# Kernel tuning notes

Measured on AMD Instinct MI355X. Metric: run time of the kernel, lower is better.

## Reference

```python
import jax, jax.numpy as jnp
import numpy as np

C, H, W = 1024, 128, 128

def setup_inputs() -> dict:
    key = jax.random.key(0)
    k1, k2 = jax.random.split(key)
    x = jax.random.normal(k1, (C, H, W), dtype=jnp.float32)
    gamma = jax.random.normal(k2, (1,), dtype=jnp.float32)
    return {"x": x, "gamma": gamma}

def reference(x, gamma):
    c, h, w = x.shape
    q = x.reshape(c, h * w)                      # (C, HW)
    energy = jnp.matmul(q, q.T)                  # (C, C)
    # negated-energy softmax: softmax(max(energy) - energy) along last dim
    energy_new = jnp.max(energy, axis=-1, keepdims=True) - energy
    attention = jax.nn.softmax(energy_new, axis=-1)
    out = jnp.matmul(attention, q).reshape(c, h, w)
    return gamma * out + x
```

## Files before the change

kernel.cpp:

```cpp
#include <hip/hip_runtime.h>
#include <hip/hip_bf16.h>

typedef unsigned short u16;
typedef float  f32x16 __attribute__((ext_vector_type(16)));
typedef short  bf16x8 __attribute__((ext_vector_type(8)));
typedef u16    u16x8  __attribute__((ext_vector_type(8)));

#define CDIM 1024
#define HW   16384

typedef const void __attribute__((address_space(1))) gvoid;
typedef void __attribute__((address_space(3))) svoid;

__device__ __forceinline__ u16 f2bf(float f) {
    unsigned u = __float_as_uint(f);
    u += 0x7fffu + ((u >> 16) & 1u);
    return (u16)(u >> 16);
}
__device__ __forceinline__ float bf2f(u16 h) { return __uint_as_float(((unsigned)h) << 16); }

__device__ __forceinline__ f32x16 mfma32(bf16x8 a, bf16x8 b, f32x16 c) {
    return __builtin_amdgcn_mfma_f32_32x32x16_bf16(a, b, c, 0, 0, 0);
}

__global__ __launch_bounds__(256) void k_convert(const float* __restrict__ x,
                                                 u16* __restrict__ hi, u16* __restrict__ lo,
                                                 u16* __restrict__ hiT)
{
    __shared__ u16 tile[64][72];
    const int pb = blockIdx.x;
    const int cb = blockIdx.y;
    const int tid = threadIdx.x;
#pragma unroll
    for (int pass = 0; pass < 4; ++pass) {
        const int i  = (tid >> 4) + (pass << 4);
        const int j4 = (tid & 15) << 2;
        const long gidx = (long)(cb * 64 + i) * HW + pb * 64 + j4;
        const float4 v = *(const float4*)(x + gidx);
        ushort4 h, l;
        h.x = f2bf(v.x); l.x = f2bf(v.x - bf2f(h.x));
        h.y = f2bf(v.y); l.y = f2bf(v.y - bf2f(h.y));
        h.z = f2bf(v.z); l.z = f2bf(v.z - bf2f(h.z));
        h.w = f2bf(v.w); l.w = f2bf(v.w - bf2f(h.w));
        *(ushort4*)(hi + gidx) = h;
        *(ushort4*)(lo + gidx) = l;
        tile[i][j4 + 0] = h.x; tile[i][j4 + 1] = h.y;
        tile[i][j4 + 2] = h.z; tile[i][j4 + 3] = h.w;
    }
    __syncthreads();
#pragma unroll
    for (int pass = 0; pass < 2; ++pass) {
        const int j  = (tid >> 3) + (pass << 5);
        const int c8 = (tid & 7) << 3;
        u16x8 v;
#pragma unroll
        for (int q = 0; q < 8; ++q) v[q] = tile[c8 + q][j];
        *(u16x8*)(hiT + (long)(pb * 64 + j) * CDIM + cb * 64 + c8) = v;
    }
}

__device__ __forceinline__ void stage_half(const u16* __restrict__ gbase, long ldg,
                                           int rowhalf, int ktile, u16* seg, int tid)
{
    const int lane = tid & 63;
    const int wv   = tid >> 6;
    const int s    = lane >> 3;
    const int r7   = (lane & 7) ^ s;
    const int col  = s << 3;
#pragma unroll
    for (int q = 0; q < 2; ++q) {
        const int j = wv + (q << 3);
        const u16* src = gbase + (long)((rowhalf << 7) + (j << 3) + r7) * ldg
                               + (ktile << 6) + col;
        __builtin_amdgcn_global_load_lds((gvoid*)src, (svoid*)(seg + (j << 9)), 16, 0, 0);
    }
}

__device__ __forceinline__ bf16x8 rd_frag(const u16* seg, int row, int kk, int lane)
{
    const int s = (kk << 1) + (lane >> 5);
    const int off = ((row >> 3) << 9) + (s << 6) + (((row & 7) ^ s) << 3);
    return *(const bf16x8*)(seg + off);
}

#define SBAR()  do { __builtin_amdgcn_sched_barrier(0); \
                     __builtin_amdgcn_s_barrier();      \
                     __builtin_amdgcn_sched_barrier(0); } while (0)

template<int EPI>
__global__ __launch_bounds__(512, 2) void k_gemm8(
    const u16* __restrict__ Amat, const u16* __restrict__ Bhi, const u16* __restrict__ Blo,
    long lda, long ldb, int kchunk, int nbn,
    float* __restrict__ C, long ldc, long csplit,
    const float* __restrict__ X, const float* __restrict__ gamma)
{
    __shared__ u16 sA[2][2][8192];
    __shared__ u16 sB[2][2][8192];

    const int tid  = threadIdx.x;
    const int lane = tid & 63;
    const int w    = tid >> 6;
    const int wm   = w >> 2;
    const int wn   = w & 3;
    const int l31  = lane & 31;

    const int ks   = blockIdx.y;
    const int nblk = gridDim.x;
    const int lin  = blockIdx.x;
    const int ti   = (lin & 7) * (nblk >> 3) + (lin >> 3);
    const int bi   = ti / nbn, bn = ti % nbn;

    const u16* Ab = Amat + (long)bi * 256 * lda + (long)ks * kchunk;
    const u16* Bb;
    if (EPI == 0) {
        const int half = nbn >> 1;
        Bb = (bn < half) ? (Bhi + (long)bn * 256 * ldb)
                         : (Blo + (long)(bn - half) * 256 * ldb);
    } else {
        Bb = Bhi + (long)bn * 256 * ldb;
    }
    Bb += (long)ks * kchunk;

    const int nkt = kchunk >> 6;

    f32x16 acc[4][2];
    {
        f32x16 z;
#pragma unroll
        for (int r = 0; r < 16; ++r) z[r] = 0.f;
#pragma unroll
        for (int f = 0; f < 4; ++f)
#pragma unroll
            for (int g = 0; g < 2; ++g) acc[f][g] = z;
    }

    stage_half(Ab, lda, 0, 0, sA[0][0], tid);
    stage_half(Ab, lda, 1, 0, sA[0][1], tid);
    stage_half(Bb, ldb, 0, 0, sB[0][0], tid);
    stage_half(Bb, ldb, 1, 0, sB[0][1], tid);

    for (int u = 0; u < nkt; ++u) {
        const int db = u & 1;

        SBAR();

        if (u + 1 < nkt) {
            stage_half(Ab, lda, 0, u + 1, sA[db ^ 1][0], tid);
            stage_half(Ab, lda, 1, u + 1, sA[db ^ 1][1], tid);
            stage_half(Bb, ldb, 0, u + 1, sB[db ^ 1][0], tid);
            stage_half(Bb, ldb, 1, u + 1, sB[db ^ 1][1], tid);
            asm volatile("s_waitcnt vmcnt(8)" ::: "memory");
        } else {
            asm volatile("s_waitcnt vmcnt(0)" ::: "memory");
        }

        bf16x8 A0f[2][4], B0f[4], B1f[4];
#pragma unroll
        for (int f = 0; f < 2; ++f)
#pragma unroll
            for (int kk = 0; kk < 4; ++kk)
                A0f[f][kk] = rd_frag(sA[db][0], wm * 64 + f * 32 + l31, kk, lane);
#pragma unroll
        for (int kk = 0; kk < 4; ++kk) B0f[kk] = rd_frag(sB[db][0], wn * 32 + l31, kk, lane);
#pragma unroll
        for (int kk = 0; kk < 4; ++kk) B1f[kk] = rd_frag(sB[db][1], wn * 32 + l31, kk, lane);

        __builtin_amdgcn_s_setprio(1);
#pragma unroll
        for (int kk = 0; kk < 4; ++kk) {
            acc[0][0] = mfma32(A0f[0][kk], B0f[kk], acc[0][0]);
            acc[1][0] = mfma32(A0f[1][kk], B0f[kk], acc[1][0]);
        }
#pragma unroll
        for (int kk = 0; kk < 4; ++kk) {
            acc[0][1] = mfma32(A0f[0][kk], B1f[kk], acc[0][1]);
            acc[1][1] = mfma32(A0f[1][kk], B1f[kk], acc[1][1]);
        }
        __builtin_amdgcn_s_setprio(0);

        bf16x8 A1f[2][4];
#pragma unroll
        for (int f = 0; f < 2; ++f)
#pragma unroll
            for (int kk = 0; kk < 4; ++kk)
                A1f[f][kk] = rd_frag(sA[db][1], wm * 64 + f * 32 + l31, kk, lane);

        __builtin_amdgcn_s_setprio(1);
#pragma unroll
        for (int kk = 0; kk < 4; ++kk) {
            acc[2][1] = mfma32(A1f[0][kk], B1f[kk], acc[2][1]);
            acc[3][1] = mfma32(A1f[1][kk], B1f[kk], acc[3][1]);
        }
#pragma unroll
        for (int kk = 0; kk < 4; ++kk) {
            acc[2][0] = mfma32(A1f[0][kk], B0f[kk], acc[2][0]);
            acc[3][0] = mfma32(A1f[1][kk], B0f[kk], acc[3][0]);
        }
        __builtin_amdgcn_s_setprio(0);
    }

    if (EPI == 0) {
        float* Cb = C + (long)ks * csplit;
#pragma unroll
        for (int f = 0; f < 4; ++f)
#pragma unroll
            for (int g = 0; g < 2; ++g)
#pragma unroll
                for (int r = 0; r < 16; ++r) {
                    const int row = bi * 256 + (f >> 1) * 128 + wm * 64 + (f & 1) * 32
                                    + (r & 3) + ((r >> 2) << 3) + ((lane >> 5) << 2);
                    const int col = bn * 256 + g * 128 + wn * 32 + l31;
                    Cb[(long)row * ldc + col] = acc[f][g][r];
                }
    } else {
        const float gm = gamma[0];
#pragma unroll
        for (int f = 0; f < 4; ++f)
#pragma unroll
            for (int g = 0; g < 2; ++g)
#pragma unroll
                for (int r = 0; r < 16; ++r) {
                    const int row = bi * 256 + (f >> 1) * 128 + wm * 64 + (f & 1) * 32
                                    + (r & 3) + ((r >> 2) << 3) + ((lane >> 5) << 2);
                    const int col = bn * 256 + g * 128 + wn * 32 + l31;
                    const long idx = (long)row * ldc + col;
                    C[idx] = gm * acc[f][g][r] + X[idx];
                }
    }
}

__global__ __launch_bounds__(256) void k_symmetrize(const float* __restrict__ E12,
                                                    float* __restrict__ Esym)
{
    __shared__ float tr[64][65];
    const int jb = blockIdx.x, ib = blockIdx.y, tid = threadIdx.x;
    float4 accv[4];
#pragma unroll
    for (int e4 = 0; e4 < 4; ++e4) {
        const int e = tid + (e4 << 8);
        const int i = e >> 4, j4 = (e & 15) << 2;
        float ax = 0, ay = 0, az = 0, aw = 0, bx = 0, by = 0, bz = 0, bw = 0;
#pragma unroll
        for (int ks = 0; ks < 8; ++ks) {
            const float* base = E12 + (long)ks * (1024 * 2048);
            float4 p1 = *(const float4*)(base + (long)(ib * 64 + i) * 2048 + jb * 64 + j4);
            float4 p2 = *(const float4*)(base + (long)(ib * 64 + i) * 2048 + 1024 + jb * 64 + j4);
            float4 p3 = *(const float4*)(base + (long)(jb * 64 + i) * 2048 + 1024 + ib * 64 + j4);
            ax += p1.x + p2.x; ay += p1.y + p2.y; az += p1.z + p2.z; aw += p1.w + p2.w;
            bx += p3.x; by += p3.y; bz += p3.z; bw += p3.w;
        }
        accv[e4] = make_float4(ax, ay, az, aw);
        tr[i][j4 + 0] = bx; tr[i][j4 + 1] = by; tr[i][j4 + 2] = bz; tr[i][j4 + 3] = bw;
    }
    __syncthreads();
#pragma unroll
    for (int e4 = 0; e4 < 4; ++e4) {
        const int e = tid + (e4 << 8);
        const int i = e >> 4, j4 = (e & 15) << 2;
        float4 o = accv[e4];
        o.x += tr[j4 + 0][i]; o.y += tr[j4 + 1][i]; o.z += tr[j4 + 2][i]; o.w += tr[j4 + 3][i];
        *(float4*)(Esym + (long)(ib * 64 + i) * CDIM + jb * 64 + j4) = o;
    }
}

__global__ __launch_bounds__(256) void k_softmax(const float* __restrict__ E, u16* __restrict__ att)
{
    __shared__ float red[4];
    __shared__ float bcast;
    const int row = blockIdx.x, tid = threadIdx.x;
    const float4 v = ((const float4*)(E + (long)row * CDIM))[tid];

    float m = fminf(fminf(v.x, v.y), fminf(v.z, v.w));
#pragma unroll
    for (int s = 32; s > 0; s >>= 1) m = fminf(m, __shfl_down(m, s));
    if ((tid & 63) == 0) red[tid >> 6] = m;
    __syncthreads();
    if (tid == 0) bcast = fminf(fminf(red[0], red[1]), fminf(red[2], red[3]));
    __syncthreads();
    m = bcast;

    const float px = expf(m - v.x), py = expf(m - v.y), pz = expf(m - v.z), pw = expf(m - v.w);
    float s4 = px + py + pz + pw;
#pragma unroll
    for (int s = 32; s > 0; s >>= 1) s4 += __shfl_down(s4, s);
    if ((tid & 63) == 0) red[tid >> 6] = s4;
    __syncthreads();
    if (tid == 0) bcast = red[0] + red[1] + red[2] + red[3];
    __syncthreads();
    const float inv = 1.0f / bcast;

    ushort4 o;
    o.x = f2bf(px * inv); o.y = f2bf(py * inv); o.z = f2bf(pz * inv); o.w = f2bf(pw * inv);
    ((ushort4*)(att + (long)row * CDIM))[tid] = o;
}

extern "C" void kernel_launch(void* const* d_in, const int* in_sizes, int n_in,
                              void* d_out, int out_size, void* d_ws, size_t ws_size,
                              hipStream_t stream)
{
    (void)in_sizes; (void)n_in; (void)out_size; (void)ws_size;
    const float* x = (const float*)d_in[0];
    const float* gamma = (const float*)d_in[1];
    float* out = (float*)d_out;
    char* ws = (char*)d_ws;

    u16*   hi   = (u16*)ws;
    u16*   lo   = (u16*)(ws + (32ull << 20));
    u16*   hiT  = (u16*)(ws + (64ull << 20));
    float* Esym = (float*)(ws + (96ull << 20));
    u16*   att  = (u16*)(ws + (100ull << 20));
    float* E12  = out;

    k_convert<<<dim3(256, 16), 256, 0, stream>>>(x, hi, lo, hiT);
    k_gemm8<0><<<dim3(32, 8), 512, 0, stream>>>(hi, hi, lo, (long)HW, (long)HW, 2048, 8,
                                                E12, 2048L, 1024L * 2048L, nullptr, nullptr);
    k_symmetrize<<<dim3(16, 16), 256, 0, stream>>>(E12, Esym);
    k_softmax<<<1024, 256, 0, stream>>>(Esym, att);
    k_gemm8<1><<<dim3(256, 1), 512, 0, stream>>>(att, hiT, nullptr, 1024L, 1024L, 1024, 64,
                                                 out, (long)HW, 0L, x, gamma);
}
```

Measured before the change: 208.0 us.

## Switch GEMM to 16x16x32 MFMA with quadrant-wise 8-phase ping-pong pipeline

Replaces the 32x32x16 bf16 MFMA tiles with 16x16x32 instructions and remaps each wave to a 128x64 output region split into four quadrants. The main loop now processes two K-tiles per iteration in eight phases: fragment reads for one quadrant are interleaved with MFMA on another, and barriers sit between phases. Global-to-LDS loads for A and B are staggered across phases so refills overlap compute. This adds many more barriers and waitcnt points, and the loop assumes an even number of K-tiles.

```diff
diff --git a/kernel.cpp b/kernel.cpp
--- a/kernel.cpp
+++ b/kernel.cpp
@@ -2,7 +2,7 @@
 #include <hip/hip_bf16.h>
 
 typedef unsigned short u16;
-typedef float  f32x16 __attribute__((ext_vector_type(16)));
+typedef float  f32x4  __attribute__((ext_vector_type(4)));
 typedef short  bf16x8 __attribute__((ext_vector_type(8)));
 typedef u16    u16x8  __attribute__((ext_vector_type(8)));
 
@@ -19,8 +19,8 @@
 }
 __device__ __forceinline__ float bf2f(u16 h) { return __uint_as_float(((unsigned)h) << 16); }
 
-__device__ __forceinline__ f32x16 mfma32(bf16x8 a, bf16x8 b, f32x16 c) {
-    return __builtin_amdgcn_mfma_f32_32x32x16_bf16(a, b, c, 0, 0, 0);
+__device__ __forceinline__ f32x4 mfma16(bf16x8 a, bf16x8 b, f32x4 c) {
+    return __builtin_amdgcn_mfma_f32_16x16x32_bf16(a, b, c, 0, 0, 0);
 }
 
 __global__ __launch_bounds__(256) void k_convert(const float* __restrict__ x,
@@ -59,6 +59,7 @@
     }
 }
 
+
 __device__ __forceinline__ void stage_half(const u16* __restrict__ gbase, long ldg,
                                            int rowhalf, int ktile, u16* seg, int tid)
 {
@@ -76,16 +77,40 @@
     }
 }
 
-__device__ __forceinline__ bf16x8 rd_frag(const u16* seg, int row, int kk, int lane)
-{
-    const int s = (kk << 1) + (lane >> 5);
+__device__ __forceinline__ bf16x8 rd_frag(const u16* seg, int row, int s)
+{
     const int off = ((row >> 3) << 9) + (s << 6) + (((row & 7) ^ s) << 3);
     return *(const bf16x8*)(seg + off);
 }
 
-#define SBAR()  do { __builtin_amdgcn_sched_barrier(0); \
-                     __builtin_amdgcn_s_barrier();      \
-                     __builtin_amdgcn_sched_barrier(0); } while (0)
+#define RD_A(BUF, QM)                                                          \
+    _Pragma("unroll") for (int mf = 0; mf < 4; ++mf)                           \
+    _Pragma("unroll") for (int k2 = 0; k2 < 2; ++k2)                           \
+        Af[mf][k2] = rd_frag(sA[BUF][wm], (QM) * 64 + mf * 16 + l15, k2 * 4 + lk);
+
+#define RD_B(BUF, QN)                                                          \
+    _Pragma("unroll") for (int nf = 0; nf < 2; ++nf)                           \
+    _Pragma("unroll") for (int k2 = 0; k2 < 2; ++k2)                           \
+        Bf[nf][k2] = rd_frag(sB[BUF][bhalf], bcolbase + (QN) * 32 + nf * 16 + l15, k2 * 4 + lk);
+
+#define MID_BAR()                                                              \
+    __builtin_amdgcn_sched_barrier(0);                                         \
+    __builtin_amdgcn_s_barrier();                                              \
+    asm volatile("s_waitcnt lgkmcnt(0)" ::: "memory");                         \
+    __builtin_amdgcn_sched_barrier(0)
+
+#define DO_MFMA(QM, QN)                                                        \
+    __builtin_amdgcn_s_setprio(1);                                             \
+    _Pragma("unroll") for (int k2 = 0; k2 < 2; ++k2)                           \
+    _Pragma("unroll") for (int mf = 0; mf < 4; ++mf)                           \
+    _Pragma("unroll") for (int nf = 0; nf < 2; ++nf)                           \
+        acc[QM][QN][mf][nf] = mfma16(Af[mf][k2], Bf[nf][k2], acc[QM][QN][mf][nf]); \
+    __builtin_amdgcn_s_setprio(0)
+
+#define END_BAR()                                                              \
+    __builtin_amdgcn_sched_barrier(0);                                         \
+    __builtin_amdgcn_s_barrier();                                              \
+    __builtin_amdgcn_sched_barrier(0)
 
 template<int EPI>
 __global__ __launch_bounds__(512, 2) void k_gemm8(
@@ -102,7 +127,10 @@
     const int w    = tid >> 6;
     const int wm   = w >> 2;
     const int wn   = w & 3;
-    const int l31  = lane & 31;
+    const int l15  = lane & 15;
+    const int lk   = lane >> 4;
+    const int bhalf    = wn >> 1;
+    const int bcolbase = (wn & 1) * 64;
 
     const int ks   = blockIdx.y;
     const int nblk = gridDim.x;
@@ -122,110 +150,114 @@
     Bb += (long)ks * kchunk;
 
     const int nkt = kchunk >> 6;
-
-    f32x16 acc[4][2];
-    {
-        f32x16 z;
-#pragma unroll
-        for (int r = 0; r < 16; ++r) z[r] = 0.f;
-#pragma unroll
-        for (int f = 0; f < 4; ++f)
-#pragma unroll
-            for (int g = 0; g < 2; ++g) acc[f][g] = z;
-    }
+    const int nit = nkt >> 1;
+
+    f32x4 acc[2][2][4][2];
+#pragma unroll
+    for (int a = 0; a < 2; ++a)
+#pragma unroll
+        for (int b = 0; b < 2; ++b)
+#pragma unroll
+            for (int c = 0; c < 4; ++c)
+#pragma unroll
+                for (int d = 0; d < 2; ++d) acc[a][b][c][d] = (f32x4){0.f, 0.f, 0.f, 0.f};
+
+    bf16x8 Af[4][2], Bf[2][2];
 
     stage_half(Ab, lda, 0, 0, sA[0][0], tid);
     stage_half(Ab, lda, 1, 0, sA[0][1], tid);
     stage_half(Bb, ldb, 0, 0, sB[0][0], tid);
     stage_half(Bb, ldb, 1, 0, sB[0][1], tid);
-
-    for (int u = 0; u < nkt; ++u) {
-        const int db = u & 1;
-
-        SBAR();
-
-        if (u + 1 < nkt) {
-            stage_half(Ab, lda, 0, u + 1, sA[db ^ 1][0], tid);
-            stage_half(Ab, lda, 1, u + 1, sA[db ^ 1][1], tid);
-            stage_half(Bb, ldb, 0, u + 1, sB[db ^ 1][0], tid);
-            stage_half(Bb, ldb, 1, u + 1, sB[db ^ 1][1], tid);
-            asm volatile("s_waitcnt vmcnt(8)" ::: "memory");
-        } else {
-            asm volatile("s_waitcnt vmcnt(0)" ::: "memory");
+    stage_half(Ab, lda, 0, 1, sA[1][0], tid);
+    stage_half(Ab, lda, 1, 1, sA[1][1], tid);
+    asm volatile("s_waitcnt vmcnt(4)" ::: "memory");
+    __builtin_amdgcn_sched_barrier(0);
+    __builtin_amdgcn_s_barrier();
+    __builtin_amdgcn_sched_barrier(0);
+
+    for (int it = 0; it < nit; ++it) {
+        const int  kt0  = it << 1, kt1 = kt0 + 1;
+        const bool lastit = (it == nit - 1);
+
+        RD_A(0, 0); RD_B(0, 0);
+        stage_half(Bb, ldb, 0, kt1, sB[1][0], tid);
+        stage_half(Bb, ldb, 1, kt1, sB[1][1], tid);
+        asm volatile("s_waitcnt lgkmcnt(8)" ::: "memory");
+        MID_BAR(); DO_MFMA(0, 0); END_BAR();
+
+        RD_B(0, 1);
+        MID_BAR(); DO_MFMA(0, 1); END_BAR();
+
+        RD_A(0, 1);
+        MID_BAR(); DO_MFMA(1, 1); END_BAR();
+
+        RD_B(0, 0);
+        if (!lastit) {
+            stage_half(Ab, lda, 0, kt0 + 2, sA[0][0], tid);
+            stage_half(Ab, lda, 1, kt0 + 2, sA[0][1], tid);
         }
-
-        bf16x8 A0f[2][4], B0f[4], B1f[4];
-#pragma unroll
-        for (int f = 0; f < 2; ++f)
-#pragma unroll
-            for (int kk = 0; kk < 4; ++kk)
-                A0f[f][kk] = rd_frag(sA[db][0], wm * 64 + f * 32 + l31, kk, lane);
-#pragma unroll
-        for (int kk = 0; kk < 4; ++kk) B0f[kk] = rd_frag(sB[db][0], wn * 32 + l31, kk, lane);
-#pragma unroll
-        for (int kk = 0; kk < 4; ++kk) B1f[kk] = rd_frag(sB[db][1], wn * 32 + l31, kk, lane);
-
-        __builtin_amdgcn_s_setprio(1);
-#pragma unroll
-        for (int kk = 0; kk < 4; ++kk) {
-            acc[0][0] = mfma32(A0f[0][kk], B0f[kk], acc[0][0]);
-            acc[1][0] = mfma32(A0f[1][kk], B0f[kk], acc[1][0]);
+        MID_BAR(); DO_MFMA(1, 0);
+        if (lastit) asm volatile("s_waitcnt vmcnt(0)" ::: "memory");
+        else        asm volatile("s_waitcnt vmcnt(4)" ::: "memory");
+        END_BAR();
+
+        RD_A(1, 0); RD_B(1, 0);
+        if (!lastit) {
+            stage_half(Bb, ldb, 0, kt0 + 2, sB[0][0], tid);
+            stage_half(Bb, ldb, 1, kt0 + 2, sB[0][1], tid);
         }
-#pragma unroll
-        for (int kk = 0; kk < 4; ++kk) {
-            acc[0][1] = mfma32(A0f[0][kk], B1f[kk], acc[0][1]);
-            acc[1][1] = mfma32(A0f[1][kk], B1f[kk], acc[1][1]);
+        asm volatile("s_waitcnt lgkmcnt(8)" ::: "memory");
+        MID_BAR(); DO_MFMA(0, 0); END_BAR();
+
+        RD_B(1, 1);
+        MID_BAR(); DO_MFMA(0, 1); END_BAR();
+
+        RD_A(1, 1);
+        MID_BAR(); DO_MFMA(1, 1); END_BAR();
+
+        RD_B(1, 0);
+        if (!lastit) {
+            stage_half(Ab, lda, 0, kt1 + 2, sA[1][0], tid);
+            stage_half(Ab, lda, 1, kt1 + 2, sA[1][1], tid);
         }
-        __builtin_amdgcn_s_setprio(0);
-
-        bf16x8 A1f[2][4];
-#pragma unroll
-        for (int f = 0; f < 2; ++f)
-#pragma unroll
-            for (int kk = 0; kk < 4; ++kk)
-                A1f[f][kk] = rd_frag(sA[db][1], wm * 64 + f * 32 + l31, kk, lane);
-
-        __builtin_amdgcn_s_setprio(1);
-#pragma unroll
-        for (int kk = 0; kk < 4; ++kk) {
-            acc[2][1] = mfma32(A1f[0][kk], B1f[kk], acc[2][1]);
-            acc[3][1] = mfma32(A1f[1][kk], B1f[kk], acc[3][1]);
-        }
-#pragma unroll
-        for (int kk = 0; kk < 4; ++kk) {
-            acc[2][0] = mfma32(A1f[0][kk], B0f[kk], acc[2][0]);
-            acc[3][0] = mfma32(A1f[1][kk], B0f[kk], acc[3][0]);
-        }
-        __builtin_amdgcn_s_setprio(0);
+        MID_BAR(); DO_MFMA(1, 0);
+        if (!lastit) asm volatile("s_waitcnt vmcnt(4)" ::: "memory");
+        END_BAR();
     }
 
     if (EPI == 0) {
         float* Cb = C + (long)ks * csplit;
 #pragma unroll
-        for (int f = 0; f < 4; ++f)
-#pragma unroll
-            for (int g = 0; g < 2; ++g)
-#pragma unroll
-                for (int r = 0; r < 16; ++r) {
-                    const int row = bi * 256 + (f >> 1) * 128 + wm * 64 + (f & 1) * 32
-                                    + (r & 3) + ((r >> 2) << 3) + ((lane >> 5) << 2);
-                    const int col = bn * 256 + g * 128 + wn * 32 + l31;
-                    Cb[(long)row * ldc + col] = acc[f][g][r];
-                }
+        for (int qm = 0; qm < 2; ++qm)
+#pragma unroll
+            for (int qn = 0; qn < 2; ++qn)
+#pragma unroll
+                for (int mf = 0; mf < 4; ++mf)
+#pragma unroll
+                    for (int nf = 0; nf < 2; ++nf)
+#pragma unroll
+                        for (int r = 0; r < 4; ++r) {
+                            const int row = bi * 256 + wm * 128 + qm * 64 + mf * 16 + lk * 4 + r;
+                            const int col = bn * 256 + wn * 64 + qn * 32 + nf * 16 + l15;
+                            Cb[(long)row * ldc + col] = acc[qm][qn][mf][nf][r];
+                        }
     } else {
         const float gm = gamma[0];
 #pragma unroll
-        for (int f = 0; f < 4; ++f)
-#pragma unroll
-            for (int g = 0; g < 2; ++g)
-#pragma unroll
-                for (int r = 0; r < 16; ++r) {
-                    const int row = bi * 256 + (f >> 1) * 128 + wm * 64 + (f & 1) * 32
-                                    + (r & 3) + ((r >> 2) << 3) + ((lane >> 5) << 2);
-                    const int col = bn * 256 + g * 128 + wn * 32 + l31;
-                    const long idx = (long)row * ldc + col;
-                    C[idx] = gm * acc[f][g][r] + X[idx];
-                }
+        for (int qm = 0; qm < 2; ++qm)
+#pragma unroll
+            for (int qn = 0; qn < 2; ++qn)
+#pragma unroll
+                for (int mf = 0; mf < 4; ++mf)
+#pragma unroll
+                    for (int nf = 0; nf < 2; ++nf)
+#pragma unroll
+                        for (int r = 0; r < 4; ++r) {
+                            const int row = bi * 256 + wm * 128 + qm * 64 + mf * 16 + lk * 4 + r;
+                            const int col = bn * 256 + wn * 64 + qn * 32 + nf * 16 + l15;
+                            const long idx = (long)row * ldc + col;
+                            C[idx] = gm * acc[qm][qn][mf][nf][r] + X[idx];
+                        }
     }
 }
 
```

Result: no change. 209.1 us (+0.5%).
